# Kernel optimization log

Hardware: AMD Instinct MI355X
Metric: run time of the kernel (lower is better)

Reference implementation:

```python
import jax, jax.numpy as jnp
import numpy as np

HIDDEN = 2048
N_HEADS = 16
N_KV = 2
HEAD_DIM = HIDDEN // N_HEADS  # 128


def setup_inputs() -> dict:
    key = jax.random.key(0)
    ks = jax.random.split(key, 9)
    s = 0.02
    kv_dim = N_KV * HEAD_DIM
    return {
        "hidden_states": jax.random.normal(ks[0], (2, 2048, HIDDEN), jnp.float32),
        "Wq": jax.random.normal(ks[1], (HIDDEN, HIDDEN), jnp.float32) * s,
        "bq": jnp.zeros((HIDDEN,), jnp.float32),
        "Wk": jax.random.normal(ks[2], (HIDDEN, kv_dim), jnp.float32) * s,
        "bk": jnp.zeros((kv_dim,), jnp.float32),
        "Wv": jax.random.normal(ks[3], (HIDDEN, kv_dim), jnp.float32) * s,
        "bv": jnp.zeros((kv_dim,), jnp.float32),
        "Wo": jax.random.normal(ks[4], (HIDDEN, HIDDEN), jnp.float32) * s,
        "bo": jnp.zeros((HIDDEN,), jnp.float32),
    }


def reference(hidden_states, Wq, bq, Wk, bk, Wv, bv, Wo, bo):
    B, S, _ = hidden_states.shape
    scaling = HEAD_DIM ** (-0.5)
    rep = N_HEADS // N_KV

    q = hidden_states @ Wq + bq                      # [B,S,H*D]
    k = hidden_states @ Wk + bk                      # [B,S,KV*D]
    v = hidden_states @ Wv + bv

    q = q.reshape(B, S, N_HEADS, HEAD_DIM) * scaling
    k = k.reshape(B, S, N_KV, HEAD_DIM)
    v = v.reshape(B, S, N_KV, HEAD_DIM)
    # repeat_interleave KV heads to match query heads (faithful to source)
    k = jnp.repeat(k, rep, axis=2)                   # [B,S,H,D]
    v = jnp.repeat(v, rep, axis=2)

    attn = jnp.einsum('bqhd,bkhd->bhqk', q, k)       # [B,H,S,S] score matrix
    attn = jax.nn.softmax(attn, axis=-1)
    out = jnp.einsum('bhqk,bkhd->bqhd', attn, v)     # [B,S,H,D]
    out = out.reshape(B, S, N_HEADS * HEAD_DIM)
    return out @ Wo + bo
```

## Files before the change

kernel.cpp:

```cpp
#include <hip/hip_runtime.h>

typedef __bf16 bf16;
typedef __bf16 bf16x4 __attribute__((ext_vector_type(4)));
typedef __bf16 bf16x8 __attribute__((ext_vector_type(8)));
typedef float  f32x4  __attribute__((ext_vector_type(4)));

#define AS1 __attribute__((address_space(1)))
#define AS3 __attribute__((address_space(3)))

__device__ __forceinline__ void gload_lds16(const void* g, void* l) {
    __builtin_amdgcn_global_load_lds((const AS1 void*)g, (AS3 void*)l, 16, 0, 0);
}

__device__ __forceinline__ int xcd_swz(int wid, int nwg) {
    return (wid & 7) * (nwg >> 3) + (wid >> 3);
}

__global__ __launch_bounds__(256) void prep(
    const float* __restrict__ X,  const float* __restrict__ Wq,
    const float* __restrict__ Wk, const float* __restrict__ Wv,
    const float* __restrict__ Wo, const float* __restrict__ bq,
    const float* __restrict__ bk, const float* __restrict__ bv,
    bf16* __restrict__ Xb, bf16* __restrict__ Wqkvt,
    bf16* __restrict__ Wot, float* __restrict__ bqkv)
{
    __shared__ float tile[32][33];
    int bid = blockIdx.x;
    if (bid < 8192) {
        int i = bid * 256 + threadIdx.x;
        float4 v = ((const float4*)X)[i];
        bf16x4 o = { (bf16)v.x, (bf16)v.y, (bf16)v.z, (bf16)v.w };
        ((bf16x4*)Xb)[i] = o;
        return;
    }
    bid -= 8192;
    const float* src; bf16* dst; int R, C, bx, by;
    if (bid < 4096)      { src = Wq; dst = Wqkvt;                      R = 2048; C = 2048; bx = bid & 63; by = bid >> 6; }
    else if (bid < 4608) { int t = bid - 4096; src = Wk; dst = Wqkvt + (size_t)2048 * 2048; R = 2048; C = 256; bx = t & 7; by = t >> 3; }
    else if (bid < 5120) { int t = bid - 4608; src = Wv; dst = Wqkvt + (size_t)2304 * 2048; R = 2048; C = 256; bx = t & 7; by = t >> 3; }
    else if (bid < 9216) { int t = bid - 5120; src = Wo; dst = Wot;    R = 2048; C = 2048; bx = t & 63; by = t >> 6; }
    else {
        int i = (bid - 9216) * 256 + threadIdx.x;
        if (i < 2048) bqkv[i] = bq[i];
        else if (i < 2304) bqkv[i] = bk[i - 2048];
        else if (i < 2560) bqkv[i] = bv[i - 2304];
        return;
    }
    int tx = threadIdx.x & 31, tg = threadIdx.x >> 5;
    int c0 = bx * 32, r0 = by * 32;
    #pragma unroll
    for (int j = tg; j < 32; j += 8)
        tile[j][tx] = src[(size_t)(r0 + j) * C + c0 + tx];
    __syncthreads();
    #pragma unroll
    for (int j = tg; j < 32; j += 8)
        dst[(size_t)(c0 + j) * R + r0 + tx] = (bf16)tile[tx][j];
}

template<int OUTBF>
__global__ __launch_bounds__(256) void gemm_bt(
    const bf16* __restrict__ A, const bf16* __restrict__ Bt,
    const float* __restrict__ bias, void* __restrict__ Cv,
    int M, int N, int K, float scale)
{
    __shared__ bf16 As[128 * 32];
    __shared__ bf16 Bs[128 * 32];
    const int tid = threadIdx.x;
    const int l = tid & 63, w = tid >> 6;
    const int wm = w >> 1, wn = w & 1;

    const int gx = N >> 7, gy = M >> 7;
    const int idx = xcd_swz(blockIdx.x + gx * blockIdx.y, gx * gy);
    const size_t colBase = (size_t)(idx % gx) * 128;
    const size_t rowBase = (size_t)(idx / gx) * 128;

    f32x4 acc[4][4] = {};

    const int srow = l >> 2;
    const int schunk = (l & 3) ^ ((l >> 3) & 3);
    const int frow = l & 15;
    const int fswz = (frow >> 1) & 3;
    const int g = l >> 4;

    const bf16* Ag = A  + (rowBase + w * 32 + srow) * (size_t)K + schunk * 8;
    const bf16* Bg = Bt + (colBase + w * 32 + srow) * (size_t)K + schunk * 8;

    for (int k0 = 0; k0 < K; k0 += 32) {
        gload_lds16(Ag + k0,                  As + (w * 32) * 32);
        gload_lds16(Ag + 16 * (size_t)K + k0, As + (w * 32 + 16) * 32);
        gload_lds16(Bg + k0,                  Bs + (w * 32) * 32);
        gload_lds16(Bg + 16 * (size_t)K + k0, Bs + (w * 32 + 16) * 32);
        __syncthreads();

        bf16x8 af[4], bfr[4];
        #pragma unroll
        for (int mi = 0; mi < 4; ++mi)
            af[mi] = *(const bf16x8*)(As + (wm * 64 + mi * 16 + frow) * 32 + ((g ^ fswz) << 3));
        #pragma unroll
        for (int ni = 0; ni < 4; ++ni)
            bfr[ni] = *(const bf16x8*)(Bs + (wn * 64 + ni * 16 + frow) * 32 + ((g ^ fswz) << 3));
        #pragma unroll
        for (int mi = 0; mi < 4; ++mi)
            #pragma unroll
            for (int ni = 0; ni < 4; ++ni)
                acc[mi][ni] = __builtin_amdgcn_mfma_f32_16x16x32_bf16(af[mi], bfr[ni], acc[mi][ni], 0, 0, 0);
        __syncthreads();
    }

    const int cr = (l >> 4) * 4;
    const int cc = l & 15;
    #pragma unroll
    for (int ni = 0; ni < 4; ++ni) {
        const int col = (int)colBase + wn * 64 + ni * 16 + cc;
        const float bv = bias[col];
        #pragma unroll
        for (int mi = 0; mi < 4; ++mi) {
            #pragma unroll
            for (int r = 0; r < 4; ++r) {
                const size_t row = rowBase + wm * 64 + mi * 16 + cr + r;
                float v = (acc[mi][ni][r] + bv) * scale;
                if (OUTBF) ((bf16*)Cv)[row * N + col] = (bf16)v;
                else       ((float*)Cv)[row * N + col] = v;
            }
        }
    }
}

__global__ __launch_bounds__(256) void gemm_qkv(
    const bf16* __restrict__ A, const bf16* __restrict__ Bt,
    const float* __restrict__ bias, bf16* __restrict__ Qb, bf16* __restrict__ Kb,
    bf16* __restrict__ VT, float qscale)
{
    constexpr int K = 2048;
    __shared__ bf16 As[128 * 32];
    __shared__ bf16 Bs[128 * 32];
    const int tid = threadIdx.x;
    const int l = tid & 63, w = tid >> 6;
    const int wm = w >> 1, wn = w & 1;

    const int idx = xcd_swz(blockIdx.x + 20 * blockIdx.y, 640);
    const size_t colBase = (size_t)(idx % 20) * 128;
    const size_t rowBase = (size_t)(idx / 20) * 128;

    f32x4 acc[4][4] = {};

    const int srow = l >> 2;
    const int schunk = (l & 3) ^ ((l >> 3) & 3);
    const int frow = l & 15;
    const int fswz = (frow >> 1) & 3;
    const int g = l >> 4;

    const bf16* Ag = A  + (rowBase + w * 32 + srow) * (size_t)K + schunk * 8;
    const bf16* Bg = Bt + (colBase + w * 32 + srow) * (size_t)K + schunk * 8;

    for (int k0 = 0; k0 < K; k0 += 32) {
        gload_lds16(Ag + k0,                  As + (w * 32) * 32);
        gload_lds16(Ag + 16 * (size_t)K + k0, As + (w * 32 + 16) * 32);
        gload_lds16(Bg + k0,                  Bs + (w * 32) * 32);
        gload_lds16(Bg + 16 * (size_t)K + k0, Bs + (w * 32 + 16) * 32);
        __syncthreads();

        bf16x8 af[4], bfr[4];
        #pragma unroll
        for (int mi = 0; mi < 4; ++mi)
            af[mi] = *(const bf16x8*)(As + (wm * 64 + mi * 16 + frow) * 32 + ((g ^ fswz) << 3));
        #pragma unroll
        for (int ni = 0; ni < 4; ++ni)
            bfr[ni] = *(const bf16x8*)(Bs + (wn * 64 + ni * 16 + frow) * 32 + ((g ^ fswz) << 3));
        #pragma unroll
        for (int mi = 0; mi < 4; ++mi)
            #pragma unroll
            for (int ni = 0; ni < 4; ++ni)
                acc[mi][ni] = __builtin_amdgcn_mfma_f32_16x16x32_bf16(af[mi], bfr[ni], acc[mi][ni], 0, 0, 0);
        __syncthreads();
    }

    const int cr = (l >> 4) * 4;
    const int cc = l & 15;
    const int cb = (int)colBase;
    #pragma unroll
    for (int ni = 0; ni < 4; ++ni) {
        const int col = cb + wn * 64 + ni * 16 + cc;
        const float bv = bias[col];
        if (cb < 2048) {
            #pragma unroll
            for (int mi = 0; mi < 4; ++mi)
                #pragma unroll
                for (int r = 0; r < 4; ++r) {
                    const size_t row = rowBase + wm * 64 + mi * 16 + cr + r;
                    Qb[row * 2048 + col] = (bf16)((acc[mi][ni][r] + bv) * qscale);
                }
        } else if (cb < 2304) {
            #pragma unroll
            for (int mi = 0; mi < 4; ++mi)
                #pragma unroll
                for (int r = 0; r < 4; ++r) {
                    const size_t row = rowBase + wm * 64 + mi * 16 + cr + r;
                    Kb[row * 256 + (col - 2048)] = (bf16)(acc[mi][ni][r] + bv);
                }
        } else {
            const int vcol = col - 2304;
            const int kvh = vcol >> 7, d = vcol & 127;
            #pragma unroll
            for (int mi = 0; mi < 4; ++mi) {
                const size_t row0 = rowBase + wm * 64 + mi * 16 + cr;
                const int bb = (int)(row0 >> 11);
                const int s  = (int)(row0 & 2047);
                const int tile = s >> 6, sp = s & 63;
                const int slot = (sp & 35) | ((sp & 8) << 1) | ((sp & 4) << 1) | ((sp & 16) >> 2);
                bf16x4 v4 = { (bf16)(acc[mi][ni][0] + bv), (bf16)(acc[mi][ni][1] + bv),
                              (bf16)(acc[mi][ni][2] + bv), (bf16)(acc[mi][ni][3] + bv) };
                *(bf16x4*)(VT + ((size_t)((bb * 2 + kvh) * 128 + d)) * 2048 + tile * 64 + slot) = v4;
            }
        }
    }
}

__global__ __launch_bounds__(256, 2) void attn_fwd(
    const bf16* __restrict__ Q, const bf16* __restrict__ Kb,
    const bf16* __restrict__ VT, bf16* __restrict__ O)
{
    constexpr int S = 2048;
    constexpr int NT = S / 64;
    extern __shared__ bf16 smem[];
    bf16* Ks = smem;
    bf16* Vs = smem + 16384;

    const int tid = threadIdx.x;
    const int l = tid & 63, w = tid >> 6;
    const int idx = xcd_swz(blockIdx.x + 16 * blockIdx.y + 256 * blockIdx.z, 512);
    const int qt = idx & 15, h = (idx >> 4) & 15, b = idx >> 8;
    const int kvh = h >> 3;
    const int lg = l >> 4, ll = l & 15;
    const int eh = (ll >> 2) & 1;

    bf16x8 qfA[4], qfB[4];
    {
        const bf16* qpA = Q + ((size_t)(b * S + qt * 128 + w * 32 + ll)) * 2048 + h * 128 + lg * 8;
        const bf16* qpB = qpA + 16 * 2048;
        #pragma unroll
        for (int j = 0; j < 4; ++j) {
            qfA[j] = *(const bf16x8*)(qpA + (j << 5));
            qfB[j] = *(const bf16x8*)(qpB + (j << 5));
        }
    }

    const bf16* Kg  = Kb + (size_t)b * S * 256 + kvh * 128;
    const bf16* VTg = VT + ((size_t)(b * 2 + kvh) * 128) * S;

    const bf16* kgA = Kg + (size_t)(w * 16 + lg) * 256 + (ll ^ lg) * 8;
    const bf16* kgB = Kg + (size_t)(w * 16 + 4 + lg) * 256 + (ll ^ (4 + lg)) * 8;
    const bf16* vgA = VTg + (size_t)(w * 32 + (l >> 3)) * S + (((l & 7) ^ ((l >> 3) & 7)) << 3);
    const int kdA = (w * 16) * 128;
    const int kdB = (w * 16 + 4) * 128;
    const int vdA = w * 2048;

    const int swz8 = (lg ^ (ll & 3)) << 3;
    const int kbE = ll * 128 + swz8 + eh * 32;
    const int kbO = ll * 128 + swz8 + (1 - eh) * 32;
    const int vbE = ll * 64 + swz8 + eh * 32;
    const int vbO = ll * 64 + swz8 + (1 - eh) * 32;

    bf16x8 vones;
    #pragma unroll
    for (int e = 0; e < 8; ++e) vones[e] = (bf16)1.0f;

    f32x4 ofA[8] = {}, ofB[8] = {};
    f32x4 olA = {}, olB = {};
    bf16x8 pA0, pA1, pB0, pB1;

#define STAGE(koff, vroff, kbuf, vslot)                                   \
    {                                                                     \
        gload_lds16(kgA + (koff),             Ks + (kbuf) * 8192 + kdA);  \
        gload_lds16(kgB + (koff),             Ks + (kbuf) * 8192 + kdB);  \
        gload_lds16(kgA + (koff) + 2048,      Ks + (kbuf) * 8192 + kdA + 1024); \
        gload_lds16(kgB + (koff) + 2048,      Ks + (kbuf) * 8192 + kdB + 1024); \
        gload_lds16(vgA + (vroff),            Vs + (vslot) * 8192 + vdA);       \
        gload_lds16(vgA + (vroff) + 8  * S,   Vs + (vslot) * 8192 + vdA + 512); \
        gload_lds16(vgA + (vroff) + 16 * S,   Vs + (vslot) * 8192 + vdA + 1024);\
        gload_lds16(vgA + (vroff) + 24 * S,   Vs + (vslot) * 8192 + vdA + 1536);\
    }

    STAGE(0, 0, 0, 0)
    __syncthreads();

    int sP = 2, sC = 0, sN = 1;
    for (int t = 0; t < NT; ++t) {
        const int buf = t & 1;
        if (t + 1 < NT) {
            const size_t ko = (size_t)(t + 1) * 64 * 256;
            const int    vo = (t + 1) * 64;
            STAGE(ko, vo, buf ^ 1, sN)
        }

        const bf16* kE = Ks + buf * 8192 + kbE;
        const bf16* kO = Ks + buf * 8192 + kbO;
        f32x4 scA[4] = {}, scB[4] = {};
        __builtin_amdgcn_s_setprio(1);
        #pragma unroll
        for (int ni = 0; ni < 4; ++ni) {
            bf16x8 k0f = *(const bf16x8*)(kE + ni * 2048);
            scA[ni] = __builtin_amdgcn_mfma_f32_16x16x32_bf16(k0f, qfA[0], scA[ni], 0, 0, 0);
            scB[ni] = __builtin_amdgcn_mfma_f32_16x16x32_bf16(k0f, qfB[0], scB[ni], 0, 0, 0);
            bf16x8 k1f = *(const bf16x8*)(kO + ni * 2048);
            scA[ni] = __builtin_amdgcn_mfma_f32_16x16x32_bf16(k1f, qfA[1], scA[ni], 0, 0, 0);
            scB[ni] = __builtin_amdgcn_mfma_f32_16x16x32_bf16(k1f, qfB[1], scB[ni], 0, 0, 0);
            bf16x8 k2f = *(const bf16x8*)(kE + ni * 2048 + 64);
            scA[ni] = __builtin_amdgcn_mfma_f32_16x16x32_bf16(k2f, qfA[2], scA[ni], 0, 0, 0);
            scB[ni] = __builtin_amdgcn_mfma_f32_16x16x32_bf16(k2f, qfB[2], scB[ni], 0, 0, 0);
            bf16x8 k3f = *(const bf16x8*)(kO + ni * 2048 + 64);
            scA[ni] = __builtin_amdgcn_mfma_f32_16x16x32_bf16(k3f, qfA[3], scA[ni], 0, 0, 0);
            scB[ni] = __builtin_amdgcn_mfma_f32_16x16x32_bf16(k3f, qfB[3], scB[ni], 0, 0, 0);
        }
        __builtin_amdgcn_s_setprio(0);

        if (t > 0) {
            const bf16* vE = Vs + sP * 8192 + vbE;
            const bf16* vO = Vs + sP * 8192 + vbO;
            __builtin_amdgcn_s_setprio(1);
            olA = __builtin_amdgcn_mfma_f32_16x16x32_bf16(pA0, vones, olA, 0, 0, 0);
            olB = __builtin_amdgcn_mfma_f32_16x16x32_bf16(pB0, vones, olB, 0, 0, 0);
            #pragma unroll
            for (int nf = 0; nf < 8; ++nf) {
                bf16x8 v0 = *(const bf16x8*)(vE + nf * 1024);
                ofA[nf] = __builtin_amdgcn_mfma_f32_16x16x32_bf16(pA0, v0, ofA[nf], 0, 0, 0);
                ofB[nf] = __builtin_amdgcn_mfma_f32_16x16x32_bf16(pB0, v0, ofB[nf], 0, 0, 0);
            }
            olA = __builtin_amdgcn_mfma_f32_16x16x32_bf16(pA1, vones, olA, 0, 0, 0);
            olB = __builtin_amdgcn_mfma_f32_16x16x32_bf16(pB1, vones, olB, 0, 0, 0);
            #pragma unroll
            for (int nf = 0; nf < 8; ++nf) {
                bf16x8 v1 = *(const bf16x8*)(vO + nf * 1024);
                ofA[nf] = __builtin_amdgcn_mfma_f32_16x16x32_bf16(pA1, v1, ofA[nf], 0, 0, 0);
                ofB[nf] = __builtin_amdgcn_mfma_f32_16x16x32_bf16(pB1, v1, ofB[nf], 0, 0, 0);
            }
            __builtin_amdgcn_s_setprio(0);
        }

        float pa[4][4], pb[4][4];
        #pragma unroll
        for (int ni = 0; ni < 4; ++ni)
            #pragma unroll
            for (int r = 0; r < 4; ++r) {
                pa[ni][r] = __builtin_exp2f(scA[ni][r]);
                pb[ni][r] = __builtin_exp2f(scB[ni][r]);
            }
        #pragma unroll
        for (int e = 0; e < 8; ++e) {
            pA0[e] = (bf16)pa[(e >> 2)][e & 3];
            pA1[e] = (bf16)pa[2 + (e >> 2)][e & 3];
            pB0[e] = (bf16)pb[(e >> 2)][e & 3];
            pB1[e] = (bf16)pb[2 + (e >> 2)][e & 3];
        }

        __syncthreads();
        int tmp = sP; sP = sC; sC = sN; sN = tmp;
    }

    {
        const bf16* vE = Vs + sP * 8192 + vbE;
        const bf16* vO = Vs + sP * 8192 + vbO;
        olA = __builtin_amdgcn_mfma_f32_16x16x32_bf16(pA0, vones, olA, 0, 0, 0);
        olB = __builtin_amdgcn_mfma_f32_16x16x32_bf16(pB0, vones, olB, 0, 0, 0);
        #pragma unroll
        for (int nf = 0; nf < 8; ++nf) {
            bf16x8 v0 = *(const bf16x8*)(vE + nf * 1024);
            ofA[nf] = __builtin_amdgcn_mfma_f32_16x16x32_bf16(pA0, v0, ofA[nf], 0, 0, 0);
            ofB[nf] = __builtin_amdgcn_mfma_f32_16x16x32_bf16(pB0, v0, ofB[nf], 0, 0, 0);
        }
        olA = __builtin_amdgcn_mfma_f32_16x16x32_bf16(pA1, vones, olA, 0, 0, 0);
        olB = __builtin_amdgcn_mfma_f32_16x16x32_bf16(pB1, vones, olB, 0, 0, 0);
        #pragma unroll
        for (int nf = 0; nf < 8; ++nf) {
            bf16x8 v1 = *(const bf16x8*)(vO + nf * 1024);
            ofA[nf] = __builtin_amdgcn_mfma_f32_16x16x32_bf16(pA1, v1, ofA[nf], 0, 0, 0);
            ofB[nf] = __builtin_amdgcn_mfma_f32_16x16x32_bf16(pB1, v1, ofB[nf], 0, 0, 0);
        }
    }

    #pragma unroll
    for (int r = 0; r < 4; ++r) {
        float invA = 1.0f / olA[r];
        float invB = 1.0f / olB[r];
        size_t rowA = (size_t)(b * S + qt * 128 + w * 32 + lg * 4 + r);
        bf16* opA = O + rowA * 2048 + h * 128 + ll;
        bf16* opB = opA + 16 * 2048;
        #pragma unroll
        for (int nf = 0; nf < 8; ++nf) {
            opA[nf * 16] = (bf16)(ofA[nf][r] * invA);
            opB[nf * 16] = (bf16)(ofB[nf][r] * invB);
        }
    }
#undef STAGE
}

extern "C" void kernel_launch(void* const* d_in, const int* in_sizes, int n_in,
                              void* d_out, int out_size, void* d_ws, size_t ws_size,
                              hipStream_t stream)
{
    const float* X  = (const float*)d_in[0];
    const float* Wq = (const float*)d_in[1];
    const float* bq = (const float*)d_in[2];
    const float* Wk = (const float*)d_in[3];
    const float* bk = (const float*)d_in[4];
    const float* Wv = (const float*)d_in[5];
    const float* bv = (const float*)d_in[6];
    const float* Wo = (const float*)d_in[7];
    const float* bo = (const float*)d_in[8];
    float* out = (float*)d_out;

    bf16* p = (bf16*)d_ws;
    bf16* Xb    = p; p += 8388608;
    bf16* Qb    = p; p += 8388608;
    bf16* Kbuf  = p; p += 1048576;
    bf16* VTb   = p; p += 1048576;
    bf16* Wqkvt = p; p += 5242880;
    bf16* Wot   = p; p += 4194304;
    float* bqkv = (float*)p; p += 5120;
    bf16* Oattn = Xb;

    const float qscale = 0.12751744f;

    (void)hipFuncSetAttribute((const void*)attn_fwd,
                              hipFuncAttributeMaxDynamicSharedMemorySize, 81920);

    prep<<<17418, 256, 0, stream>>>(X, Wq, Wk, Wv, Wo, bq, bk, bv,
                                    Xb, Wqkvt, Wot, bqkv);

    gemm_qkv<<<dim3(20, 32), 256, 0, stream>>>(Xb, Wqkvt, bqkv, Qb, Kbuf, VTb, qscale);

    attn_fwd<<<dim3(16, 16, 2), 256, 81920, stream>>>(Qb, Kbuf, VTb, Oattn);

    gemm_bt<0><<<dim3(16, 32), 256, 0, stream>>>(Oattn, Wot, bo, out, 4096, 2048, 2048, 1.0f);
}
```

Before: 194.0 us.

## Load V fragments directly from global into registers instead of via LDS

Result: slower. 259.9 us (+34.0%).

```diff
diff --git a/kernel.cpp b/kernel.cpp
--- a/kernel.cpp
+++ b/kernel.cpp
@@ -222,9 +222,7 @@
 {
     constexpr int S = 2048;
     constexpr int NT = S / 64;
-    extern __shared__ bf16 smem[];
-    bf16* Ks = smem;
-    bf16* Vs = smem + 16384;
+    __shared__ bf16 Ks[2 * 64 * 128];
 
     const int tid = threadIdx.x;
     const int l = tid & 63, w = tid >> 6;
@@ -250,16 +248,14 @@
 
     const bf16* kgA = Kg + (size_t)(w * 16 + lg) * 256 + (ll ^ lg) * 8;
     const bf16* kgB = Kg + (size_t)(w * 16 + 4 + lg) * 256 + (ll ^ (4 + lg)) * 8;
-    const bf16* vgA = VTg + (size_t)(w * 32 + (l >> 3)) * S + (((l & 7) ^ ((l >> 3) & 7)) << 3);
     const int kdA = (w * 16) * 128;
     const int kdB = (w * 16 + 4) * 128;
-    const int vdA = w * 2048;
 
     const int swz8 = (lg ^ (ll & 3)) << 3;
     const int kbE = ll * 128 + swz8 + eh * 32;
     const int kbO = ll * 128 + swz8 + (1 - eh) * 32;
-    const int vbE = ll * 64 + swz8 + eh * 32;
-    const int vbO = ll * 64 + swz8 + (1 - eh) * 32;
+
+    const bf16* vgB = VTg + (size_t)ll * S + lg * 8;
 
     bf16x8 vones;
     #pragma unroll
@@ -268,30 +264,22 @@
     f32x4 ofA[8] = {}, ofB[8] = {};
     f32x4 olA = {}, olB = {};
     bf16x8 pA0, pA1, pB0, pB1;
-
-#define STAGE(koff, vroff, kbuf, vslot)                                   \
-    {                                                                     \
-        gload_lds16(kgA + (koff),             Ks + (kbuf) * 8192 + kdA);  \
-        gload_lds16(kgB + (koff),             Ks + (kbuf) * 8192 + kdB);  \
-        gload_lds16(kgA + (koff) + 2048,      Ks + (kbuf) * 8192 + kdA + 1024); \
-        gload_lds16(kgB + (koff) + 2048,      Ks + (kbuf) * 8192 + kdB + 1024); \
-        gload_lds16(vgA + (vroff),            Vs + (vslot) * 8192 + vdA);       \
-        gload_lds16(vgA + (vroff) + 8  * S,   Vs + (vslot) * 8192 + vdA + 512); \
-        gload_lds16(vgA + (vroff) + 16 * S,   Vs + (vslot) * 8192 + vdA + 1024);\
-        gload_lds16(vgA + (vroff) + 24 * S,   Vs + (vslot) * 8192 + vdA + 1536);\
-    }
-
-    STAGE(0, 0, 0, 0)
+    bf16x8 vr0[8], vr1[8];
+
+#define STAGEK(koff, kbuf)                                                      \
+    {                                                                           \
+        gload_lds16(kgA + (koff),        Ks + (kbuf) * 8192 + kdA);             \
+        gload_lds16(kgB + (koff),        Ks + (kbuf) * 8192 + kdB);             \
+        gload_lds16(kgA + (koff) + 2048, Ks + (kbuf) * 8192 + kdA + 1024);      \
+        gload_lds16(kgB + (koff) + 2048, Ks + (kbuf) * 8192 + kdB + 1024);      \
+    }
+
+    STAGEK(0, 0)
     __syncthreads();
 
-    int sP = 2, sC = 0, sN = 1;
     for (int t = 0; t < NT; ++t) {
         const int buf = t & 1;
-        if (t + 1 < NT) {
-            const size_t ko = (size_t)(t + 1) * 64 * 256;
-            const int    vo = (t + 1) * 64;
-            STAGE(ko, vo, buf ^ 1, sN)
-        }
+        if (t + 1 < NT) STAGEK((size_t)(t + 1) * 64 * 256, buf ^ 1)
 
         const bf16* kE = Ks + buf * 8192 + kbE;
         const bf16* kO = Ks + buf * 8192 + kbO;
@@ -315,26 +303,31 @@
         __builtin_amdgcn_s_setprio(0);
 
         if (t > 0) {
-            const bf16* vE = Vs + sP * 8192 + vbE;
-            const bf16* vO = Vs + sP * 8192 + vbO;
             __builtin_amdgcn_s_setprio(1);
             olA = __builtin_amdgcn_mfma_f32_16x16x32_bf16(pA0, vones, olA, 0, 0, 0);
             olB = __builtin_amdgcn_mfma_f32_16x16x32_bf16(pB0, vones, olB, 0, 0, 0);
             #pragma unroll
             for (int nf = 0; nf < 8; ++nf) {
-                bf16x8 v0 = *(const bf16x8*)(vE + nf * 1024);
-                ofA[nf] = __builtin_amdgcn_mfma_f32_16x16x32_bf16(pA0, v0, ofA[nf], 0, 0, 0);
-                ofB[nf] = __builtin_amdgcn_mfma_f32_16x16x32_bf16(pB0, v0, ofB[nf], 0, 0, 0);
+                ofA[nf] = __builtin_amdgcn_mfma_f32_16x16x32_bf16(pA0, vr0[nf], ofA[nf], 0, 0, 0);
+                ofB[nf] = __builtin_amdgcn_mfma_f32_16x16x32_bf16(pB0, vr0[nf], ofB[nf], 0, 0, 0);
             }
             olA = __builtin_amdgcn_mfma_f32_16x16x32_bf16(pA1, vones, olA, 0, 0, 0);
             olB = __builtin_amdgcn_mfma_f32_16x16x32_bf16(pB1, vones, olB, 0, 0, 0);
             #pragma unroll
             for (int nf = 0; nf < 8; ++nf) {
-                bf16x8 v1 = *(const bf16x8*)(vO + nf * 1024);
-                ofA[nf] = __builtin_amdgcn_mfma_f32_16x16x32_bf16(pA1, v1, ofA[nf], 0, 0, 0);
-                ofB[nf] = __builtin_amdgcn_mfma_f32_16x16x32_bf16(pB1, v1, ofB[nf], 0, 0, 0);
+                ofA[nf] = __builtin_amdgcn_mfma_f32_16x16x32_bf16(pA1, vr1[nf], ofA[nf], 0, 0, 0);
+                ofB[nf] = __builtin_amdgcn_mfma_f32_16x16x32_bf16(pB1, vr1[nf], ofB[nf], 0, 0, 0);
             }
             __builtin_amdgcn_s_setprio(0);
+        }
+
+        {
+            const bf16* vsrc = vgB + t * 64;
+            #pragma unroll
+            for (int nf = 0; nf < 8; ++nf) {
+                vr0[nf] = *(const bf16x8*)(vsrc + (size_t)nf * 32768);
+                vr1[nf] = *(const bf16x8*)(vsrc + (size_t)nf * 32768 + 32);
+            }
         }
 
         float pa[4][4], pb[4][4];
@@ -354,27 +347,22 @@
         }
 
         __syncthreads();
-        int tmp = sP; sP = sC; sC = sN; sN = tmp;
     }
 
     {
-        const bf16* vE = Vs + sP * 8192 + vbE;
-        const bf16* vO = Vs + sP * 8192 + vbO;
         olA = __builtin_amdgcn_mfma_f32_16x16x32_bf16(pA0, vones, olA, 0, 0, 0);
         olB = __builtin_amdgcn_mfma_f32_16x16x32_bf16(pB0, vones, olB, 0, 0, 0);
         #pragma unroll
         for (int nf = 0; nf < 8; ++nf) {
-            bf16x8 v0 = *(const bf16x8*)(vE + nf * 1024);
-            ofA[nf] = __builtin_amdgcn_mfma_f32_16x16x32_bf16(pA0, v0, ofA[nf], 0, 0, 0);
-            ofB[nf] = __builtin_amdgcn_mfma_f32_16x16x32_bf16(pB0, v0, ofB[nf], 0, 0, 0);
+            ofA[nf] = __builtin_amdgcn_mfma_f32_16x16x32_bf16(pA0, vr0[nf], ofA[nf], 0, 0, 0);
+            ofB[nf] = __builtin_amdgcn_mfma_f32_16x16x32_bf16(pB0, vr0[nf], ofB[nf], 0, 0, 0);
         }
         olA = __builtin_amdgcn_mfma_f32_16x16x32_bf16(pA1, vones, olA, 0, 0, 0);
         olB = __builtin_amdgcn_mfma_f32_16x16x32_bf16(pB1, vones, olB, 0, 0, 0);
         #pragma unroll
         for (int nf = 0; nf < 8; ++nf) {
-            bf16x8 v1 = *(const bf16x8*)(vO + nf * 1024);
-            ofA[nf] = __builtin_amdgcn_mfma_f32_16x16x32_bf16(pA1, v1, ofA[nf], 0, 0, 0);
-            ofB[nf] = __builtin_amdgcn_mfma_f32_16x16x32_bf16(pB1, v1, ofB[nf], 0, 0, 0);
+            ofA[nf] = __builtin_amdgcn_mfma_f32_16x16x32_bf16(pA1, vr1[nf], ofA[nf], 0, 0, 0);
+            ofB[nf] = __builtin_amdgcn_mfma_f32_16x16x32_bf16(pB1, vr1[nf], ofB[nf], 0, 0, 0);
         }
     }
 
@@ -391,7 +379,7 @@
             opB[nf * 16] = (bf16)(ofB[nf][r] * invB);
         }
     }
-#undef STAGE
+#undef STAGEK
 }
 
 extern "C" void kernel_launch(void* const* d_in, const int* in_sizes, int n_in,
@@ -421,15 +409,12 @@
 
     const float qscale = 0.12751744f;
 
-    (void)hipFuncSetAttribute((const void*)attn_fwd,
-                              hipFuncAttributeMaxDynamicSharedMemorySize, 81920);
-
     prep<<<17418, 256, 0, stream>>>(X, Wq, Wk, Wv, Wo, bq, bk, bv,
                                     Xb, Wqkvt, Wot, bqkv);
 
     gemm_qkv<<<dim3(20, 32), 256, 0, stream>>>(Xb, Wqkvt, bqkv, Qb, Kbuf, VTb, qscale);
 
-    attn_fwd<<<dim3(16, 16, 2), 256, 81920, stream>>>(Qb, Kbuf, VTb, Oattn);
+    attn_fwd<<<dim3(16, 16, 2), 256, 0, stream>>>(Qb, Kbuf, VTb, Oattn);
 
     gemm_bt<0><<<dim3(16, 32), 256, 0, stream>>>(Oattn, Wot, bo, out, 4096, 2048, 2048, 1.0f);
 }
```
